# Kernel tuning notes

Hardware: AMD Instinct MI355X
Metric: run time of the kernel (lower is better)

The kernel has to match this reference:

```python
import jax, jax.numpy as jnp
import numpy as np

B, L, D, H = 8, 2048, 1024, 16
FACTOR = 3


def setup_inputs() -> dict:
    key = jax.random.key(0)
    ks = jax.random.split(key, 11)
    s = 0.02
    mk = lambda k, shp: jax.random.normal(k, shp, dtype=jnp.float32)
    return {
        "queries": mk(ks[0], (B, L, D)),
        "keys": mk(ks[1], (B, L, D)),
        "values": mk(ks[2], (B, L, D)),
        "Wq": mk(ks[3], (D, D)) * s, "bq": jnp.zeros((D,), jnp.float32),
        "Wk": mk(ks[4], (D, D)) * s, "bk": jnp.zeros((D,), jnp.float32),
        "Wv": mk(ks[5], (D, D)) * s, "bv": jnp.zeros((D,), jnp.float32),
        "Wo": mk(ks[6], (D, D)) * s, "bo": jnp.zeros((D,), jnp.float32),
    }


def reference(queries, keys, values, Wq, bq, Wk, bk, Wv, bv, Wo, bo):
    b, length, d = queries.shape
    h = H
    e = d // h
    q = (queries @ Wq + bq).reshape(b, length, h, e)
    k = (keys @ Wk + bk).reshape(b, length, h, e)
    v = (values @ Wv + bv).reshape(b, length, h, e)

    # [B, H, E, L] layout for FFT along time
    qf = jnp.fft.rfft(q.transpose(0, 2, 3, 1), axis=-1)
    kf = jnp.fft.rfft(k.transpose(0, 2, 3, 1), axis=-1)
    corr = jnp.fft.irfft(qf * jnp.conj(kf), n=length, axis=-1)  # [B,H,E,L]

    vperm = v.transpose(0, 2, 3, 1)  # [B,H,E,L]
    top_k = int(FACTOR * np.log(length))  # static: 22 for L=2048
    weights, delay = jax.lax.top_k(corr, top_k)          # [B,H,E,K]
    temp_corr = jax.nn.softmax(weights, axis=-1)         # [B,H,E,K]

    idx0 = jnp.arange(length)  # [L]
    agg = jnp.zeros_like(vperm)
    # small fixed loop over top-k delays (mirrors original structure)
    for i in range(top_k):
        # faithful to source: indices wrapped mod 8 (original code quirk)
        td = (idx0[None, None, None, :] + delay[..., i:i + 1]) % 8  # [B,H,E,L]
        pattern = jnp.take_along_axis(vperm, td, axis=-1)
        agg = agg + pattern * temp_corr[..., i:i + 1]

    result = agg.transpose(0, 3, 1, 2).reshape(b, length, d)  # [B,L,D]
    out = result @ Wo + bo
    return (out, corr.transpose(0, 3, 1, 2))
```

## Files before the change

### kernel.cpp

```cpp
#include <hip/hip_runtime.h>
#include <cstdint>
#include <cstddef>


#define TOPK 22

typedef __attribute__((ext_vector_type(8))) short short8;
typedef __attribute__((ext_vector_type(4))) float f32x4;

__device__ __forceinline__ float bf2f(unsigned short u) {
  union { unsigned int i; float f; } w;
  w.i = ((unsigned int)u) << 16;
  return w.f;
}
__device__ __forceinline__ unsigned short f2bf(float f) {
  union { float f; unsigned int i; } w;
  w.f = f;
  unsigned int x = w.i;
  x += 0x7fffu + ((x >> 16) & 1u);
  return (unsigned short)(x >> 16);
}

__device__ __forceinline__ void gload_lds16(const void* g, void* l) {
  __builtin_amdgcn_global_load_lds(
      (const __attribute__((address_space(1))) unsigned int*)g,
      (__attribute__((address_space(3))) unsigned int*)l, 16, 0, 0);
}

__device__ __forceinline__ float2 make2(float x, float y) { float2 r; r.x = x; r.y = y; return r; }
__device__ __forceinline__ float2 cadd(float2 a, float2 b) { return make2(a.x + b.x, a.y + b.y); }
__device__ __forceinline__ float2 csub(float2 a, float2 b) { return make2(a.x - b.x, a.y - b.y); }
__device__ __forceinline__ float2 cmul(float2 a, float2 b) {
  return make2(a.x * b.x - a.y * b.y, a.x * b.y + a.y * b.x);
}

__device__ __forceinline__ int cfi(int u) { return 2 * u + (((u) >> 5) << 1); }

template <bool INV>
__device__ __forceinline__ void dft8(float2 (&v)[8]) {
  const float C = 0.70710678118654752f;
  float2 s0 = cadd(v[0], v[4]), s1 = csub(v[0], v[4]);
  float2 s2 = cadd(v[2], v[6]), s3 = csub(v[2], v[6]);
  float2 E0 = cadd(s0, s2), E2 = csub(s0, s2);
  float2 E1, E3;
  if (!INV) { E1 = make2(s1.x + s3.y, s1.y - s3.x); E3 = make2(s1.x - s3.y, s1.y + s3.x); }
  else      { E1 = make2(s1.x - s3.y, s1.y + s3.x); E3 = make2(s1.x + s3.y, s1.y - s3.x); }
  float2 q0 = cadd(v[1], v[5]), q1 = csub(v[1], v[5]);
  float2 q2 = cadd(v[3], v[7]), q3 = csub(v[3], v[7]);
  float2 O0 = cadd(q0, q2), O2 = csub(q0, q2);
  float2 O1, O3;
  if (!INV) { O1 = make2(q1.x + q3.y, q1.y - q3.x); O3 = make2(q1.x - q3.y, q1.y + q3.x); }
  else      { O1 = make2(q1.x - q3.y, q1.y + q3.x); O3 = make2(q1.x + q3.y, q1.y - q3.x); }
  float2 T0 = O0, T1, T2, T3;
  if (!INV) {
    T1 = make2(C * (O1.x + O1.y), C * (O1.y - O1.x));
    T2 = make2(O2.y, -O2.x);
    T3 = make2(C * (O3.y - O3.x), -C * (O3.x + O3.y));
  } else {
    T1 = make2(C * (O1.x - O1.y), C * (O1.x + O1.y));
    T2 = make2(-O2.y, O2.x);
    T3 = make2(-C * (O3.x + O3.y), C * (O3.x - O3.y));
  }
  v[0] = cadd(E0, T0); v[4] = csub(E0, T0);
  v[1] = cadd(E1, T1); v[5] = csub(E1, T1);
  v[2] = cadd(E2, T2); v[6] = csub(E2, T2);
  v[3] = cadd(E3, T3); v[7] = csub(E3, T3);
}

template <bool INV>
__device__ __forceinline__ void dft4(float2 (&v)[4]) {
  float2 s0 = cadd(v[0], v[2]), s1 = csub(v[0], v[2]);
  float2 s2 = cadd(v[1], v[3]), s3 = csub(v[1], v[3]);
  v[0] = cadd(s0, s2); v[2] = csub(s0, s2);
  if (!INV) { v[1] = make2(s1.x + s3.y, s1.y - s3.x); v[3] = make2(s1.x - s3.y, s1.y + s3.x); }
  else      { v[1] = make2(s1.x - s3.y, s1.y + s3.x); v[3] = make2(s1.x + s3.y, s1.y - s3.x); }
}

template <int NS, bool INV>
__device__ __forceinline__ void stage8(const float* __restrict__ src,
                                       float* __restrict__ dst, int tid) {
  float2 v[8];
#pragma unroll
  for (int m = 0; m < 8; ++m)
    v[m] = *reinterpret_cast<const float2*>(src + cfi(tid + (m << 8)));
  if constexpr (NS > 1) {
    const int r = tid & (NS - 1);
    const float rev = (INV ? (1.0f / (8 * NS)) : (-1.0f / (8 * NS))) * (float)r;
    float2 w1; w1.x = __builtin_amdgcn_cosf(rev); w1.y = __builtin_amdgcn_sinf(rev);
    const float2 w2 = cmul(w1, w1);
    const float2 w3 = cmul(w2, w1);
    const float2 w4 = cmul(w2, w2);
    const float2 w5 = cmul(w4, w1);
    const float2 w6 = cmul(w4, w2);
    const float2 w7 = cmul(w4, w3);
    v[1] = cmul(v[1], w1); v[2] = cmul(v[2], w2); v[3] = cmul(v[3], w3);
    v[4] = cmul(v[4], w4); v[5] = cmul(v[5], w5); v[6] = cmul(v[6], w6);
    v[7] = cmul(v[7], w7);
  }
  dft8<INV>(v);
  const int r2 = tid & (NS - 1);
  const int d = ((tid & ~(NS - 1)) << 3) | r2;
#pragma unroll
  for (int m = 0; m < 8; ++m)
    *reinterpret_cast<float2*>(dst + cfi(d + m * NS)) = v[m];
}

__device__ __forceinline__ void radix_pick(const unsigned int* h,
                                           unsigned int* sb,
                                           unsigned int need, int tid) {
  if (tid < 64) {
    const unsigned int c0 = h[4 * tid + 0];
    const unsigned int c1 = h[4 * tid + 1];
    const unsigned int c2 = h[4 * tid + 2];
    const unsigned int c3 = h[4 * tid + 3];
    const unsigned int g = c0 + c1 + c2 + c3;
    unsigned int S = g;
#pragma unroll
    for (int off = 1; off < 64; off <<= 1) {
      const unsigned int o = __shfl_down(S, off);
      if (tid + off < 64) S += o;
    }
    unsigned int A = S - g;
    int pick = -1;
    unsigned int nn = 0;
    const unsigned int cc[4] = {c0, c1, c2, c3};
#pragma unroll
    for (int j = 3; j >= 0; --j) {
      if (pick < 0) {
        if (A < need && need <= A + cc[j]) { pick = j; nn = need - A; }
        else A += cc[j];
      }
    }
    if (pick >= 0) { sb[0] = (unsigned int)(4 * tid + pick); sb[1] = nn; }
  }
}

__global__ __launch_bounds__(256) void conv_bf16(
    const float* __restrict__ q, const float* __restrict__ k,
    unsigned short* __restrict__ qb, unsigned short* __restrict__ kb) {
  const size_t nchunks = (size_t)16777216 / 8;
  for (size_t i = (size_t)blockIdx.x * 256 + threadIdx.x; i < 2 * nchunks;
       i += (size_t)gridDim.x * 256) {
    const bool isq = i < nchunks;
    const float* src = isq ? q : k;
    unsigned short* dst = isq ? qb : kb;
    const size_t c = isq ? i : i - nchunks;
    const float4 a0 = reinterpret_cast<const float4*>(src)[c * 2];
    const float4 a1 = reinterpret_cast<const float4*>(src)[c * 2 + 1];
    uint4 p;
    p.x = f2bf(a0.x) | ((unsigned int)f2bf(a0.y) << 16);
    p.y = f2bf(a0.z) | ((unsigned int)f2bf(a0.w) << 16);
    p.z = f2bf(a1.x) | ((unsigned int)f2bf(a1.y) << 16);
    p.w = f2bf(a1.z) | ((unsigned int)f2bf(a1.w) << 16);
    reinterpret_cast<uint4*>(dst)[c] = p;
  }
}

__global__ __launch_bounds__(256) void transpose_w(
    const float* __restrict__ Wq, const float* __restrict__ Wk,
    unsigned short* __restrict__ WqT, unsigned short* __restrict__ WkT) {
  __shared__ unsigned short T[64][72];
  const float* src = blockIdx.z ? Wk : Wq;
  unsigned short* dst = blockIdx.z ? WkT : WqT;
  const int k0 = blockIdx.x * 64;
  const int n0 = blockIdx.y * 64;
  const int c = threadIdx.x & 63;
  const int r0 = threadIdx.x >> 6;
#pragma unroll
  for (int p = 0; p < 16; ++p) {
    const int r = r0 + 4 * p;
    T[c][r] = f2bf(src[(size_t)(k0 + r) * 1024 + n0 + c]);
  }
  __syncthreads();
#pragma unroll
  for (int p = 0; p < 16; ++p) {
    const int nn = r0 + 4 * p;
    dst[(size_t)(n0 + nn) * 1024 + k0 + c] = T[nn][c];
  }
}

__global__ __launch_bounds__(256, 2) void gemm_qk_bf(
    const unsigned short* __restrict__ Abf,
    const unsigned short* __restrict__ WT,
    const float* __restrict__ bias,
    unsigned short* __restrict__ outT) {
  __shared__ __align__(16) unsigned short smem[16384];
  unsigned short* As = smem;
  unsigned short* Bs = smem + 4096;

  const int tid = threadIdx.x;
  const int lane = tid & 63;
  const int w = tid >> 6;
  const int wr = w >> 1, wc = w & 1;
  const int m0 = blockIdx.x * 128;
  const int n0 = blockIdx.y * 128;
  const int l15 = lane & 15;
  const int quad = lane >> 4;

  const int srow = lane >> 2;
  const int scol = (lane & 3) * 8;

  f32x4 acc[4][4];
#pragma unroll
  for (int i = 0; i < 4; ++i)
#pragma unroll
    for (int j = 0; j < 4; ++j)
#pragma unroll
      for (int r = 0; r < 4; ++r) acc[i][j][r] = 0.f;

  for (int k0 = 0; k0 < 1024; k0 += 32) {
    __syncthreads();
    const unsigned short* Ab = Abf + (size_t)m0 * 1024 + k0;
    const unsigned short* Bb = WT + (size_t)n0 * 1024 + k0;
#pragma unroll
    for (int i = 0; i < 2; ++i) {
      const int cc = w * 2 + i;
      const int row = cc * 16 + srow;
      gload_lds16(Ab + (size_t)row * 1024 + scol, As + cc * 512);
      gload_lds16(Bb + (size_t)row * 1024 + scol, Bs + cc * 512);
    }
    __syncthreads();

    short8 af[4], bfr[4];
#pragma unroll
    for (int mt = 0; mt < 4; ++mt)
      af[mt] = *reinterpret_cast<const short8*>(As + (wr * 64 + mt * 16 + l15) * 32 + quad * 8);
#pragma unroll
    for (int nt = 0; nt < 4; ++nt)
      bfr[nt] = *reinterpret_cast<const short8*>(Bs + (wc * 64 + nt * 16 + l15) * 32 + quad * 8);
#pragma unroll
    for (int mt = 0; mt < 4; ++mt)
#pragma unroll
      for (int nt = 0; nt < 4; ++nt)
        acc[mt][nt] = __builtin_amdgcn_mfma_f32_16x16x32_bf16(af[mt], bfr[nt], acc[mt][nt], 0, 0, 0);
  }

  __syncthreads();
  unsigned short* Cs = smem;
#pragma unroll
  for (int nt = 0; nt < 4; ++nt) {
    const int n_local = wc * 64 + nt * 16 + l15;
    const float bv = bias[n0 + n_local];
#pragma unroll
    for (int mt = 0; mt < 4; ++mt) {
      const int mbase = wr * 64 + mt * 16 + quad * 4;
#pragma unroll
      for (int r = 0; r < 4; ++r)
        Cs[n_local * 128 + mbase + r] = f2bf(acc[mt][nt][r] + bv);
    }
  }
  __syncthreads();

  const int b = m0 >> 11;
  const int l0 = m0 & 2047;
  for (int it = tid; it < 2048; it += 256) {
    const int rowi = it >> 4;
    const int ci = it & 15;
    uint4 v = *reinterpret_cast<const uint4*>(Cs + rowi * 128 + ci * 8);
    *reinterpret_cast<uint4*>(outT + (size_t)(b * 1024 + n0 + rowi) * 2048 + l0 + ci * 8) = v;
  }
}

__global__ __launch_bounds__(256) void vsmall_kernel(
    const float* __restrict__ values,
    const float* __restrict__ Wv,
    const float* __restrict__ bv,
    float* __restrict__ out) {
  __shared__ float xr[1024];
  const int m = blockIdx.x;
  const int b = m >> 3, t = m & 7;
  const float* row = values + ((size_t)b * 2048 + t) * 1024;
  for (int i = threadIdx.x; i < 1024; i += 256) xr[i] = row[i];
  __syncthreads();
  const int n = blockIdx.y * 256 + threadIdx.x;
  float acc = 0.f;
#pragma unroll 8
  for (int k = 0; k < 1024; ++k) acc += xr[k] * Wv[(size_t)k * 1024 + n];
  out[(size_t)m * 1024 + n] = acc + bv[n];
}

__global__ __launch_bounds__(256, 4) void corr_topk(
    const unsigned short* __restrict__ Qt,
    const unsigned short* Kt,
    const float* __restrict__ vsmall,
    unsigned short* corrOut,
    float* __restrict__ agg) {
  __shared__ __align__(16) float bufA[4224];
  __shared__ __align__(16) float bufB[4224];

  const int tid = threadIdx.x;
  const int lane = tid & 63;
  const int wv = tid >> 6;
  const int s = blockIdx.x;
  const size_t base = (size_t)s * 2048;

  unsigned int* hist = reinterpret_cast<unsigned int*>(bufB);
  float* bins = bufB + 1024;
  float* wred = bufB + 1032;
  int* ired = reinterpret_cast<int*>(bufB + 1036);
  unsigned int* sb = reinterpret_cast<unsigned int*>(bufB + 1040);

  {
    float2 v[8];
#pragma unroll
    for (int m = 0; m < 8; ++m) {
      const int u = tid + (m << 8);
      v[m] = make2(bf2f(Qt[base + u]), bf2f(Kt[base + u]));
    }
    dft8<false>(v);
    const int d = tid << 3;
#pragma unroll
    for (int m = 0; m < 8; ++m)
      *reinterpret_cast<float2*>(bufA + cfi(d + m)) = v[m];
  }
  __syncthreads();

  stage8<8, false>(bufA, bufB, tid);
  __syncthreads();
  stage8<64, false>(bufB, bufA, tid);
  __syncthreads();

  {
#pragma unroll
    for (int h = 0; h < 2; ++h) {
      const int j = tid + (h << 8);
      float2 v[4];
#pragma unroll
      for (int m = 0; m < 4; ++m)
        v[m] = *reinterpret_cast<const float2*>(bufA + cfi(j + (m << 9)));
      const float rev = -(1.0f / 2048.0f) * (float)j;
      float2 w1; w1.x = __builtin_amdgcn_cosf(rev); w1.y = __builtin_amdgcn_sinf(rev);
      const float2 w2 = cmul(w1, w1);
      const float2 w3 = cmul(w2, w1);
      v[1] = cmul(v[1], w1); v[2] = cmul(v[2], w2); v[3] = cmul(v[3], w3);
      dft4<false>(v);
#pragma unroll
      for (int m = 0; m < 4; ++m)
        *reinterpret_cast<float2*>(bufB + cfi(j + (m << 9))) = v[m];
    }
  }
  __syncthreads();

  {
    float2 v[8];
    const float ks = 1.0f / 8192.0f;
#pragma unroll
    for (int m = 0; m < 8; ++m) {
      const int u = tid + (m << 8);
      const int ub = (2048 - u) & 2047;
      const float2 Av = *reinterpret_cast<const float2*>(bufB + cfi(u));
      const float2 Bv = *reinterpret_cast<const float2*>(bufB + cfi(ub));
      const float Px = Av.x + Bv.x, Py = Av.y - Bv.y;
      const float Qx = Av.x - Bv.x, Qy = -Av.y - Bv.y;
      const float X1 = (Px * Qx - Py * Qy) * ks;
      const float Y1 = (Px * Qy + Py * Qx) * ks;
      v[m] = make2(-Y1, X1);
    }
    dft8<true>(v);
    const int d = tid << 3;
#pragma unroll
    for (int m = 0; m < 8; ++m)
      *reinterpret_cast<float2*>(bufA + cfi(d + m)) = v[m];
  }
  __syncthreads();

  stage8<8, true>(bufA, bufB, tid);
  __syncthreads();
  stage8<64, true>(bufB, bufA, tid);
  __syncthreads();

  float cval[8];
#pragma unroll
  for (int h = 0; h < 2; ++h) {
    const int j = tid + (h << 8);
    float2 v0 = *reinterpret_cast<const float2*>(bufA + cfi(j));
    float2 v1 = *reinterpret_cast<const float2*>(bufA + cfi(j + 512));
    float2 v2 = *reinterpret_cast<const float2*>(bufA + cfi(j + 1024));
    float2 v3 = *reinterpret_cast<const float2*>(bufA + cfi(j + 1536));
    const float rev = (1.0f / 2048.0f) * (float)j;
    float2 w1; w1.x = __builtin_amdgcn_cosf(rev); w1.y = __builtin_amdgcn_sinf(rev);
    const float2 w2 = cmul(w1, w1);
    const float2 w3 = cmul(w2, w1);
    const float2 t1 = cmul(v1, w1);
    const float2 t3 = cmul(v3, w3);
    const float t2x = v2.x * w2.x - v2.y * w2.y;
    cval[h]     = v0.x + t1.x + t2x + t3.x;
    cval[h + 2] = v0.x - t1.y - t2x + t3.y;
    cval[h + 4] = v0.x - t1.x + t2x - t3.x;
    cval[h + 6] = v0.x + t1.y - t2x - t3.y;
  }

#pragma unroll
  for (int i = 0; i < 8; ++i)
    corrOut[base + (size_t)(tid + (i << 8))] = f2bf(cval[i]);

  unsigned int key[8];
#pragma unroll
  for (int i = 0; i < 8; ++i) {
    union { float f; unsigned int u; } cvt;
    cvt.f = cval[i];
    const unsigned int b = cvt.u;
    key[i] = (b & 0x80000000u) ? ~b : (b | 0x80000000u);
  }

#pragma unroll
  for (int q = 0; q < 4; ++q) hist[(q << 8) + tid] = 0u;
  if (tid < 8) bins[tid] = 0.f;
  {
    float vm = cval[0];
#pragma unroll
    for (int i = 1; i < 8; ++i) vm = fmaxf(vm, cval[i]);
#pragma unroll
    for (int off = 32; off > 0; off >>= 1) vm = fmaxf(vm, __shfl_down(vm, off));
    if (lane == 0) wred[wv] = vm;
  }
  __syncthreads();
  const float mx = fmaxf(fmaxf(wred[0], wred[1]), fmaxf(wred[2], wred[3]));

  unsigned int prefix = 0;
  unsigned int need = TOPK;
#pragma unroll
  for (int i = 0; i < 8; ++i) atomicAdd(&hist[key[i] >> 24], 1u);
  __syncthreads();
  radix_pick(hist, sb, need, tid);
  __syncthreads();
  prefix = sb[0]; need = sb[1];
#pragma unroll
  for (int i = 0; i < 8; ++i)
    if ((key[i] >> 24) == prefix) atomicAdd(&hist[256 + ((key[i] >> 16) & 255u)], 1u);
  __syncthreads();
  radix_pick(hist + 256, sb, need, tid);
  __syncthreads();
  prefix = (prefix << 8) | sb[0]; need = sb[1];
#pragma unroll
  for (int i = 0; i < 8; ++i)
    if ((key[i] >> 16) == prefix) atomicAdd(&hist[512 + ((key[i] >> 8) & 255u)], 1u);
  __syncthreads();
  radix_pick(hist + 512, sb, need, tid);
  __syncthreads();
  prefix = (prefix << 8) | sb[0]; need = sb[1];
#pragma unroll
  for (int i = 0; i < 8; ++i)
    if ((key[i] >> 8) == prefix) atomicAdd(&hist[768 + (key[i] & 255u)], 1u);
  __syncthreads();
  radix_pick(hist + 768, sb, need, tid);
  __syncthreads();
  const unsigned int T = (prefix << 8) | sb[0];
  const unsigned int takeEq = sb[1];

  unsigned int eqm = 0, selEq = 0;
#pragma unroll
  for (int i = 0; i < 8; ++i)
    if (key[i] == T) eqm |= (1u << i);
  for (unsigned int it2 = 0; it2 < takeEq; ++it2) {
    int mi = 0x7fffffff;
#pragma unroll
    for (int i = 0; i < 8; ++i)
      if (eqm & (1u << i)) mi = min(mi, tid + (i << 8));
#pragma unroll
    for (int off = 32; off > 0; off >>= 1) {
      const int o = __shfl_down(mi, off);
      if (lane + off < 64) mi = min(mi, o);
    }
    if (lane == 0) ired[wv] = mi;
    __syncthreads();
    const int gm = min(min(ired[0], ired[1]), min(ired[2], ired[3]));
#pragma unroll
    for (int i = 0; i < 8; ++i)
      if ((tid + (i << 8)) == gm) { selEq |= (1u << i); eqm &= ~(1u << i); }
    if (it2 + 1 < takeEq) __syncthreads();
  }

  float esum = 0.f;
#pragma unroll
  for (int i = 0; i < 8; ++i) {
    const bool sel = (key[i] > T) || ((selEq >> i) & 1u);
    if (sel) esum += __expf(cval[i] - mx);
  }
  if (esum > 0.f) atomicAdd(&bins[tid & 7], esum);
  __syncthreads();

  if (tid < 8) {
    const float ssum = bins[0] + bins[1] + bins[2] + bins[3] +
                       bins[4] + bins[5] + bins[6] + bins[7];
    const int b = s >> 10, n = s & 1023;
    float a = 0.f;
#pragma unroll
    for (int c = 0; c < 8; ++c)
      a += bins[c] * vsmall[(size_t)(b * 8 + ((tid + c) & 7)) * 1024 + n];
    agg[(size_t)(b * 8 + tid) * 1024 + n] = a / ssum;
  }
}

__global__ __launch_bounds__(256) void osmall_kernel(
    const float* __restrict__ aggin,
    const float* __restrict__ Wo,
    const float* __restrict__ bo,
    float* __restrict__ out) {
  __shared__ float xr[1024];
  const int m = blockIdx.x;
  const float* row = aggin + (size_t)m * 1024;
  for (int i = threadIdx.x; i < 1024; i += 256) xr[i] = row[i];
  __syncthreads();
  const int n = blockIdx.y * 256 + threadIdx.x;
  float acc = 0.f;
#pragma unroll 8
  for (int k = 0; k < 1024; ++k) acc += xr[k] * Wo[(size_t)k * 1024 + n];
  out[(size_t)m * 1024 + n] = acc + bo[n];
}

__global__ __launch_bounds__(256) void corr_transpose(
    const unsigned short* __restrict__ corrWs,
    float* __restrict__ out1) {
  __shared__ unsigned short T[64][72];
  const int bb = blockIdx.z;
  const int l0 = blockIdx.x * 64;
  const int n0 = blockIdx.y * 64;
  const int c = threadIdx.x & 63;
  const int r0 = threadIdx.x >> 6;
#pragma unroll
  for (int p = 0; p < 16; ++p) {
    const int r = r0 + 4 * p;
    T[c][r] = corrWs[(size_t)(bb * 1024 + n0 + r) * 2048 + l0 + c];
  }
  __syncthreads();
#pragma unroll
  for (int p = 0; p < 16; ++p) {
    const int ll = r0 + 4 * p;
    out1[(size_t)(bb * 2048 + l0 + ll) * 1024 + n0 + c] = bf2f(T[ll][c]);
  }
}

__global__ __launch_bounds__(256) void bcast_out(
    const float* __restrict__ outSmall,
    float* __restrict__ out0) {
  const size_t i4 = (size_t)blockIdx.x * 256 + threadIdx.x;
  const size_t basee = i4 * 4;
  const int n = (int)(basee & 1023);
  const int l = (int)((basee >> 10) & 2047);
  const int b = (int)(basee >> 21);
  const float4 v = *reinterpret_cast<const float4*>(outSmall + ((size_t)(b * 8 + (l & 7)) << 10) + n);
  *reinterpret_cast<float4*>(out0 + basee) = v;
}

extern "C" void kernel_launch(void* const* d_in, const int* in_sizes, int n_in,
                              void* d_out, int out_size, void* d_ws, size_t ws_size,
                              hipStream_t stream) {
  const float* queries = (const float*)d_in[0];
  const float* keys    = (const float*)d_in[1];
  const float* values  = (const float*)d_in[2];
  const float* Wq = (const float*)d_in[3];
  const float* bq = (const float*)d_in[4];
  const float* Wk = (const float*)d_in[5];
  const float* bk = (const float*)d_in[6];
  const float* Wv = (const float*)d_in[7];
  const float* bv = (const float*)d_in[8];
  const float* Wo = (const float*)d_in[9];
  const float* bo = (const float*)d_in[10];

  char* ws = (char*)d_ws;
  unsigned short* WqT = (unsigned short*)(ws);
  unsigned short* WkT = (unsigned short*)(ws + (2u << 20));
  unsigned short* Qt  = (unsigned short*)(ws + (4u << 20));
  float* vsmall   = (float*)(ws + (36u << 20));
  float* aggbuf   = (float*)(ws + (36u << 20) + (256u << 10));
  float* outSmall = (float*)(ws + (36u << 20) + (512u << 10));

  float* out0 = (float*)d_out;
  float* out1 = out0 + (size_t)16777216;
  unsigned short* Kt = (unsigned short*)d_out;
  unsigned short* corrWs = Kt;
  unsigned short* Qbf = (unsigned short*)out1;
  unsigned short* Kbf = Qbf + (size_t)16777216;

  conv_bf16<<<4096, 256, 0, stream>>>(queries, keys, Qbf, Kbf);
  transpose_w<<<dim3(16, 16, 2), 256, 0, stream>>>(Wq, Wk, WqT, WkT);
  gemm_qk_bf<<<dim3(128, 8), 256, 0, stream>>>(Qbf, WqT, bq, Qt);
  gemm_qk_bf<<<dim3(128, 8), 256, 0, stream>>>(Kbf, WkT, bk, Kt);
  vsmall_kernel<<<dim3(64, 4), 256, 0, stream>>>(values, Wv, bv, vsmall);
  corr_topk<<<8192, 256, 0, stream>>>(Qt, Kt, vsmall, corrWs, aggbuf);
  osmall_kernel<<<dim3(64, 4), 256, 0, stream>>>(aggbuf, Wo, bo, outSmall);
  corr_transpose<<<dim3(32, 16, 8), 256, 0, stream>>>(corrWs, out1);
  bcast_out<<<16384, 256, 0, stream>>>(outSmall, out0);
}
```

Baseline: 632.5 us.

## Double-buffer LDS in Q/K projection GEMM and remap workgroups for XCD locality

The Q/K projection GEMM now uses two LDS buffers, prefetching the next K-slice with global_load_lds while MFMAs run on the current one, which removes one barrier per iteration. The grid is flattened to 1D and block IDs are swizzled so consecutive workgroups on the same XCD share B tiles. Launch bounds rise to 4 blocks per CU. The aim is to hide global load latency and improve L2 reuse, at the cost of tighter register limits that could cause spills.

Result: no change. 644.7 us (+1.9%).

```diff
diff --git a/kernel.cpp b/kernel.cpp
--- a/kernel.cpp
+++ b/kernel.cpp
@@ -179,27 +179,29 @@
   }
 }
 
-__global__ __launch_bounds__(256, 2) void gemm_qk_bf(
+__global__ __launch_bounds__(256, 4) void gemm_qk_bf(
     const unsigned short* __restrict__ Abf,
     const unsigned short* __restrict__ WT,
     const float* __restrict__ bias,
     unsigned short* __restrict__ outT) {
   __shared__ __align__(16) unsigned short smem[16384];
-  unsigned short* As = smem;
-  unsigned short* Bs = smem + 4096;
 
   const int tid = threadIdx.x;
   const int lane = tid & 63;
   const int w = tid >> 6;
   const int wr = w >> 1, wc = w & 1;
-  const int m0 = blockIdx.x * 128;
-  const int n0 = blockIdx.y * 128;
+  const int wg = blockIdx.x;
+  const int sid = ((wg & 7) << 7) | (wg >> 3);
+  const int m0 = (sid & 127) << 7;
+  const int n0 = (sid >> 7) << 7;
   const int l15 = lane & 15;
   const int quad = lane >> 4;
-
   const int srow = lane >> 2;
   const int scol = (lane & 3) * 8;
 
+  const unsigned short* Abase = Abf + (size_t)m0 * 1024;
+  const unsigned short* Bbase = WT + (size_t)n0 * 1024;
+
   f32x4 acc[4][4];
 #pragma unroll
   for (int i = 0; i < 4; ++i)
@@ -208,34 +210,53 @@
 #pragma unroll
       for (int r = 0; r < 4; ++r) acc[i][j][r] = 0.f;
 
-  for (int k0 = 0; k0 < 1024; k0 += 32) {
-    __syncthreads();
-    const unsigned short* Ab = Abf + (size_t)m0 * 1024 + k0;
-    const unsigned short* Bb = WT + (size_t)n0 * 1024 + k0;
+  {
+    unsigned short* As = smem;
+    unsigned short* Bs = smem + 4096;
 #pragma unroll
     for (int i = 0; i < 2; ++i) {
       const int cc = w * 2 + i;
       const int row = cc * 16 + srow;
-      gload_lds16(Ab + (size_t)row * 1024 + scol, As + cc * 512);
-      gload_lds16(Bb + (size_t)row * 1024 + scol, Bs + cc * 512);
+      gload_lds16(Abase + (size_t)row * 1024 + scol, As + cc * 512);
+      gload_lds16(Bbase + (size_t)row * 1024 + scol, Bs + cc * 512);
+    }
+  }
+  __syncthreads();
+
+  int cur = 0;
+  for (int t = 0; t < 32; ++t) {
+    if (t < 31) {
+      const int k0 = (t + 1) * 32;
+      unsigned short* As = smem + ((cur ^ 1) << 13);
+      unsigned short* Bs = As + 4096;
+#pragma unroll
+      for (int i = 0; i < 2; ++i) {
+        const int cc = w * 2 + i;
+        const int row = cc * 16 + srow;
+        gload_lds16(Abase + (size_t)row * 1024 + k0 + scol, As + cc * 512);
+        gload_lds16(Bbase + (size_t)row * 1024 + k0 + scol, Bs + cc * 512);
+      }
+    }
+    {
+      const unsigned short* As = smem + (cur << 13);
+      const unsigned short* Bs = As + 4096;
+      short8 af[4], bfr[4];
+#pragma unroll
+      for (int mt = 0; mt < 4; ++mt)
+        af[mt] = *reinterpret_cast<const short8*>(As + (wr * 64 + mt * 16 + l15) * 32 + quad * 8);
+#pragma unroll
+      for (int nt = 0; nt < 4; ++nt)
+        bfr[nt] = *reinterpret_cast<const short8*>(Bs + (wc * 64 + nt * 16 + l15) * 32 + quad * 8);
+#pragma unroll
+      for (int mt = 0; mt < 4; ++mt)
+#pragma unroll
+        for (int nt = 0; nt < 4; ++nt)
+          acc[mt][nt] = __builtin_amdgcn_mfma_f32_16x16x32_bf16(af[mt], bfr[nt], acc[mt][nt], 0, 0, 0);
     }
     __syncthreads();
-
-    short8 af[4], bfr[4];
-#pragma unroll
-    for (int mt = 0; mt < 4; ++mt)
-      af[mt] = *reinterpret_cast<const short8*>(As + (wr * 64 + mt * 16 + l15) * 32 + quad * 8);
-#pragma unroll
-    for (int nt = 0; nt < 4; ++nt)
-      bfr[nt] = *reinterpret_cast<const short8*>(Bs + (wc * 64 + nt * 16 + l15) * 32 + quad * 8);
-#pragma unroll
-    for (int mt = 0; mt < 4; ++mt)
-#pragma unroll
-      for (int nt = 0; nt < 4; ++nt)
-        acc[mt][nt] = __builtin_amdgcn_mfma_f32_16x16x32_bf16(af[mt], bfr[nt], acc[mt][nt], 0, 0, 0);
-  }
-
-  __syncthreads();
+    cur ^= 1;
+  }
+
   unsigned short* Cs = smem;
 #pragma unroll
   for (int nt = 0; nt < 4; ++nt) {
@@ -575,8 +596,8 @@
 
   conv_bf16<<<4096, 256, 0, stream>>>(queries, keys, Qbf, Kbf);
   transpose_w<<<dim3(16, 16, 2), 256, 0, stream>>>(Wq, Wk, WqT, WkT);
-  gemm_qk_bf<<<dim3(128, 8), 256, 0, stream>>>(Qbf, WqT, bq, Qt);
-  gemm_qk_bf<<<dim3(128, 8), 256, 0, stream>>>(Kbf, WkT, bk, Kt);
+  gemm_qk_bf<<<1024, 256, 0, stream>>>(Qbf, WqT, bq, Qt);
+  gemm_qk_bf<<<1024, 256, 0, stream>>>(Kbf, WkT, bk, Kt);
   vsmall_kernel<<<dim3(64, 4), 256, 0, stream>>>(values, Wv, bv, vsmall);
   corr_topk<<<8192, 256, 0, stream>>>(Qt, Kt, vsmall, corrWs, aggbuf);
   osmall_kernel<<<dim3(64, 4), 256, 0, stream>>>(aggbuf, Wo, bo, outSmall);
```
